# Kernel tuning notes

Hardware: AMD Instinct MI355X
Metric: run time of the kernel (lower is better)

The kernel has to match this reference:

```python
import jax, jax.numpy as jnp
import numpy as np

DIM = 512
HIDDEN = 1024
NUM_EXPERTS = 8
TOP_K = 2
BALANCE_LOSS_WEIGHT = 0.01


def setup_inputs() -> dict:
    key = jax.random.key(0)
    ks = jax.random.split(key, 6)
    B, S = 4, 8192
    x = jax.random.normal(ks[0], (B, S, DIM), dtype=jnp.float32)
    # Linear params (stored already transposed for x @ W convenience)
    scale_in = 1.0 / np.sqrt(DIM)
    scale_hid = 1.0 / np.sqrt(HIDDEN)
    gate_w = jax.random.uniform(ks[1], (DIM, NUM_EXPERTS), jnp.float32, -scale_in, scale_in)
    w1 = jax.random.uniform(ks[2], (NUM_EXPERTS, DIM, HIDDEN), jnp.float32, -scale_in, scale_in)
    b1 = jax.random.uniform(ks[3], (NUM_EXPERTS, HIDDEN), jnp.float32, -scale_in, scale_in)
    w2 = jax.random.uniform(ks[4], (NUM_EXPERTS, HIDDEN, DIM), jnp.float32, -scale_hid, scale_hid)
    b2 = jax.random.uniform(ks[5], (NUM_EXPERTS, DIM), jnp.float32, -scale_hid, scale_hid)
    return {"x": x, "gate_w": gate_w, "w1": w1, "b1": b1, "w2": w2, "b2": b2}


def reference(x, gate_w, w1, b1, w2, b2):
    B, S, D = x.shape
    T = B * S
    E = gate_w.shape[1]
    flat_x = x.reshape(T, D)

    # Gating (eval mode: no noise)
    gate_logits = flat_x @ gate_w                      # [T, E]
    gates = jax.nn.softmax(gate_logits, axis=-1)
    top_k_gates, top_k_indices = jax.lax.top_k(gates, TOP_K)
    top_k_gates = top_k_gates / jnp.sum(top_k_gates, axis=-1, keepdims=True)

    rows = jnp.arange(T)[:, None]
    # Per-token combine weight for each expert (0 if not selected)
    combine_w = jnp.zeros((T, E), flat_x.dtype).at[rows, top_k_indices].add(top_k_gates)
    # Load-balance loss (indices are discrete -> constant mask)
    expert_mask = jnp.zeros((T, E), flat_x.dtype).at[rows, top_k_indices].set(1.0)
    expert_usage = expert_mask.sum(0) / T
    balance_loss = jnp.mean((expert_usage - 1.0 / E) ** 2) * E * BALANCE_LOSS_WEIGHT

    # Expert MLPs; unselected tokens have combine weight 0 so contribute nothing,
    # matching the original masked gather/scatter math exactly.
    out = jnp.zeros_like(flat_x)
    for e in range(E):  # small fixed expert count
        h = jax.nn.gelu(flat_x @ w1[e] + b1[e], approximate=False)  # [T, HIDDEN]
        out = out + (h @ w2[e] + b2[e]) * combine_w[:, e:e + 1]
    return out.reshape(B, S, D), balance_loss
```

## Files before the change

### kernel.cpp

```cpp
#include <hip/hip_runtime.h>
#include <stdint.h>

#define T_TOK 32768
#define DDIM 512
#define HID 1024
#define NEXP 8

typedef _Float16 f16;
typedef _Float16 f16x8 __attribute__((ext_vector_type(8)));
typedef _Float16 f16x4 __attribute__((ext_vector_type(4)));
typedef float f32x4 __attribute__((ext_vector_type(4)));

__device__ __forceinline__ void gload_lds16(const void* g, void* l) {
  __builtin_amdgcn_global_load_lds(
      (__attribute__((address_space(1))) void*)g,
      (__attribute__((address_space(3))) void*)l, 16, 0, 0);
}

__global__ void k_cvt_x(const float* __restrict__ x, f16* __restrict__ xh) {
  int i = blockIdx.x * blockDim.x + threadIdx.x;
  float4 v = ((const float4*)x)[i];
  f16x4 o = {(f16)v.x, (f16)v.y, (f16)v.z, (f16)v.w};
  ((f16x4*)xh)[i] = o;
}

__global__ void k_transpose(const float* __restrict__ W, f16* __restrict__ Wt,
                            const int K, const int N) {
  __shared__ float tile[64][65];
  const int e = blockIdx.z;
  const float* Wb = W + (size_t)e * K * N;
  f16* Wtb = Wt + (size_t)e * K * N;
  const int k0 = blockIdx.x * 64, n0 = blockIdx.y * 64;
  const int tr = threadIdx.x >> 2;
  const int tc = (threadIdx.x & 3) * 16;
#pragma unroll
  for (int j = 0; j < 16; j += 4) {
    float4 v = *(const float4*)&Wb[(size_t)(k0 + tr) * N + n0 + tc + j];
    tile[tr][tc + j + 0] = v.x; tile[tr][tc + j + 1] = v.y;
    tile[tr][tc + j + 2] = v.z; tile[tr][tc + j + 3] = v.w;
  }
  __syncthreads();
  f16x8 t0, t1;
#pragma unroll
  for (int j = 0; j < 8; ++j) {
    t0[j] = (f16)tile[tc + j][tr];
    t1[j] = (f16)tile[tc + 8 + j][tr];
  }
  *(f16x8*)&Wtb[(size_t)(n0 + tr) * K + k0 + tc] = t0;
  *(f16x8*)&Wtb[(size_t)(n0 + tr) * K + k0 + tc + 8] = t1;
}

__global__ void k_gate(const float* __restrict__ x, const float* __restrict__ gw,
                       int* __restrict__ route_e, float* __restrict__ route_w,
                       int* __restrict__ cnt) {
  __shared__ int scnt[NEXP];
  const int tid = threadIdx.x, lane = tid & 63, wv = tid >> 6;
  if (tid < NEXP) scnt[tid] = 0;
  __syncthreads();

  float ga[4][8], gb[4][8];
#pragma unroll
  for (int j = 0; j < 4; ++j) {
    const int r0 = lane * 4 + j;
    const int r1 = 256 + lane * 4 + j;
    float4 q0 = *(const float4*)&gw[r0 * 8];
    float4 q1 = *(const float4*)&gw[r0 * 8 + 4];
    ga[j][0] = q0.x; ga[j][1] = q0.y; ga[j][2] = q0.z; ga[j][3] = q0.w;
    ga[j][4] = q1.x; ga[j][5] = q1.y; ga[j][6] = q1.z; ga[j][7] = q1.w;
    q0 = *(const float4*)&gw[r1 * 8];
    q1 = *(const float4*)&gw[r1 * 8 + 4];
    gb[j][0] = q0.x; gb[j][1] = q0.y; gb[j][2] = q0.z; gb[j][3] = q0.w;
    gb[j][4] = q1.x; gb[j][5] = q1.y; gb[j][6] = q1.z; gb[j][7] = q1.w;
  }

  const int tbase = blockIdx.x * 32 + wv * 8;
  for (int it = 0; it < 8; ++it) {
    const int t = tbase + it;
    const float4 A = *(const float4*)&x[(size_t)t * DDIM + lane * 4];
    const float4 B = *(const float4*)&x[(size_t)t * DDIM + 256 + lane * 4];
    float p[8];
#pragma unroll
    for (int e = 0; e < 8; ++e) {
      p[e] = A.x * ga[0][e] + A.y * ga[1][e] + A.z * ga[2][e] + A.w * ga[3][e] +
             B.x * gb[0][e] + B.y * gb[1][e] + B.z * gb[2][e] + B.w * gb[3][e];
    }
#pragma unroll
    for (int off = 32; off >= 1; off >>= 1) {
#pragma unroll
      for (int e = 0; e < 8; ++e) p[e] += __shfl_xor(p[e], off);
    }
    if (lane == 0) {
      int e1 = 0;
#pragma unroll
      for (int e = 1; e < 8; ++e) if (p[e] > p[e1]) e1 = e;
      int e2 = (e1 == 0) ? 1 : 0;
#pragma unroll
      for (int e = 0; e < 8; ++e) if (e != e1 && p[e] > p[e2]) e2 = e;
      const float wa = 1.0f / (1.0f + expf(p[e2] - p[e1]));
      route_e[t] = e1 | (e2 << 8);
      route_w[t] = wa;
      atomicAdd(&scnt[e1], 1);
      atomicAdd(&scnt[e2], 1);
    }
  }
  __syncthreads();
  if (tid < NEXP) atomicAdd(&cnt[tid], scnt[tid]);
}

__global__ void k_scan(const int* __restrict__ cnt, int* __restrict__ base,
                       int* __restrict__ cursor, float* __restrict__ out_loss) {
  if (threadIdx.x == 0) {
    int b = 0;
    float loss = 0.0f;
    for (int e = 0; e < NEXP; ++e) {
      base[e] = b;
      cursor[e] = b;
      b += cnt[e];
      float u = (float)cnt[e] / (float)T_TOK - 0.125f;
      loss += u * u;
    }
    *out_loss = loss * 0.01f;
  }
}

__global__ void k_scatter(const int* __restrict__ route_e, const float* __restrict__ route_w,
                          int* __restrict__ cursor, int* __restrict__ tok_slot,
                          float* __restrict__ wgt_slot) {
  const int t = blockIdx.x * blockDim.x + threadIdx.x;
  const int lane = threadIdx.x & 63;
  const int re = route_e[t];
  const float wa = route_w[t];
  const int e1 = re & 0xff, e2 = re >> 8;
#pragma unroll
  for (int e = 0; e < NEXP; ++e) {
    unsigned long long m = __ballot(e1 == e);
    if (m) {
      const int leader = __ffsll(m) - 1;
      int b0 = 0;
      if (lane == leader) b0 = atomicAdd(&cursor[e], __popcll(m));
      b0 = __shfl(b0, leader);
      if (e1 == e) {
        const int pos = b0 + __popcll(m & ((1ull << lane) - 1));
        tok_slot[pos] = t;
        wgt_slot[pos] = wa;
      }
    }
    m = __ballot(e2 == e);
    if (m) {
      const int leader = __ffsll(m) - 1;
      int b0 = 0;
      if (lane == leader) b0 = atomicAdd(&cursor[e], __popcll(m));
      b0 = __shfl(b0, leader);
      if (e2 == e) {
        const int pos = b0 + __popcll(m & ((1ull << lane) - 1));
        tok_slot[pos] = t;
        wgt_slot[pos] = 1.0f - wa;
      }
    }
  }
}

#define STAGE_TILE(k0_, As_, Bs_)                                   \
  do {                                                              \
    _Pragma("unroll") for (int i = 0; i < 4; ++i) {                 \
      gload_lds16(aSrc[i] + (k0_), &(As_)[wv * 2048 + i * 512]);    \
      gload_lds16(bSrc[i] + (k0_), &(Bs_)[wv * 2048 + i * 512]);    \
    }                                                               \
  } while (0)

#define COMPUTE_TILE(As_, Bs_)                                                    \
  do {                                                                            \
    _Pragma("unroll") for (int kb = 0; kb < 2; ++kb) {                            \
      f16x8 af[8], bf[4];                                                         \
      _Pragma("unroll") for (int mf = 0; mf < 8; ++mf) {                          \
        const int row = wm * 128 + mf * 16 + l15;                                 \
        af[mf] = *(const f16x8*)&(As_)[row * 64 + (((kb * 4 + g) ^ (row & 7)) * 8)]; \
      }                                                                           \
      _Pragma("unroll") for (int nf = 0; nf < 4; ++nf) {                          \
        const int row = wn * 64 + nf * 16 + l15;                                  \
        bf[nf] = *(const f16x8*)&(Bs_)[row * 64 + (((kb * 4 + g) ^ (row & 7)) * 8)]; \
      }                                                                           \
      _Pragma("unroll") for (int mf = 0; mf < 8; ++mf)                            \
        _Pragma("unroll") for (int nf = 0; nf < 4; ++nf)                          \
          acc[mf][nf] =                                                           \
              __builtin_amdgcn_mfma_f32_16x16x32_f16(af[mf], bf[nf], acc[mf][nf], 0, 0, 0); \
    }                                                                             \
  } while (0)

__global__ __launch_bounds__(512, 2) void k_mlp1(
    const f16* __restrict__ xh, const f16* __restrict__ w1t,
    const float* __restrict__ b1, f16* __restrict__ h,
    const int* __restrict__ tok_slot, const int* __restrict__ base,
    const int* __restrict__ cnt, const int hc, const int c0) {
  const int lid = blockIdx.x;
  const int e = lid & 7;
  const int q = lid >> 3;
  const int mt = q & 63;
  const int nt = q >> 6;
  const int ne = cnt[e];
  const int n0 = nt * 256;
  const int sbase = base[e];
  const int shi = sbase + ne;

  __shared__ f16 As0[256 * 64];
  __shared__ f16 Bs0[256 * 64];
  __shared__ f16 As1[256 * 64];
  __shared__ f16 Bs1[256 * 64];

  const int tid = threadIdx.x;
  const int lane = tid & 63;
  const int wv = tid >> 6;
  const int wm = wv >> 2, wn = wv & 3;
  const int g = lane >> 4;
  const int l15 = lane & 15;

  for (int m0 = mt * 256; m0 < ne; m0 += 64 * 256) {
    const int slot0 = sbase + m0;

    const f16* aSrc[4];
    const f16* bSrc[4];
#pragma unroll
    for (int i = 0; i < 4; ++i) {
      const int row = wv * 32 + i * 8 + (lane >> 3);
      const int sw = ((lane & 7) ^ (lane >> 3)) * 8;
      int slot = slot0 + row;
      slot = (slot <= shi - 1) ? slot : (shi - 1);
      const int tok = tok_slot[slot];
      aSrc[i] = xh + (size_t)tok * DDIM + sw;
      bSrc[i] = w1t + (size_t)(e * HID + c0 + n0 + row) * DDIM + sw;
    }

    f32x4 acc[8][4];
#pragma unroll
    for (int a = 0; a < 8; ++a)
#pragma unroll
      for (int b = 0; b < 4; ++b) { f32x4 z = {0.f, 0.f, 0.f, 0.f}; acc[a][b] = z; }

    const int NT = DDIM / 64;
    STAGE_TILE(0, As0, Bs0);
    __syncthreads();
    for (int t = 0; t < NT; t += 2) {
      if (t + 1 < NT) STAGE_TILE((t + 1) * 64, As1, Bs1);
      COMPUTE_TILE(As0, Bs0);
      __syncthreads();
      if (t + 2 < NT) STAGE_TILE((t + 2) * 64, As0, Bs0);
      COMPUTE_TILE(As1, Bs1);
      __syncthreads();
    }

#pragma unroll
    for (int mf = 0; mf < 8; ++mf) {
#pragma unroll
      for (int r = 0; r < 4; ++r) {
        const int row = wm * 128 + mf * 16 + g * 4 + r;
        const int slot = slot0 + row;
        if (slot >= shi) continue;
#pragma unroll
        for (int nf = 0; nf < 4; ++nf) {
          const int col = wn * 64 + nf * 16 + l15;
          float v = acc[mf][nf][r] + b1[e * HID + c0 + n0 + col];
          v = 0.5f * v * (1.0f + erff(v * 0.70710678118654752f));
          h[(size_t)slot * hc + n0 + col] = (f16)v;
        }
      }
    }
  }
}

__global__ __launch_bounds__(512, 2) void k_mlp2(
    const f16* __restrict__ h, const f16* __restrict__ w2t,
    const float* __restrict__ b2, float* __restrict__ out,
    const int* __restrict__ tok_slot, const float* __restrict__ wgt_slot,
    const int* __restrict__ base, const int* __restrict__ cnt,
    const int hc, const int c0) {
  const int lid = blockIdx.x;
  const int e = lid & 7;
  const int q = lid >> 3;
  const int mt = q & 63;
  const int nt = q >> 6;
  const int ne = cnt[e];
  const int n0 = nt * 256;
  const int sbase = base[e];
  const int shi = sbase + ne;

  __shared__ f16 As0[256 * 64];
  __shared__ f16 Bs0[256 * 64];
  __shared__ f16 As1[256 * 64];
  __shared__ f16 Bs1[256 * 64];

  const int tid = threadIdx.x;
  const int lane = tid & 63;
  const int wv = tid >> 6;
  const int wm = wv >> 2, wn = wv & 3;
  const int g = lane >> 4;
  const int l15 = lane & 15;

  for (int m0 = mt * 256; m0 < ne; m0 += 64 * 256) {
    const int slot0 = sbase + m0;

    const f16* aSrc[4];
    const f16* bSrc[4];
#pragma unroll
    for (int i = 0; i < 4; ++i) {
      const int row = wv * 32 + i * 8 + (lane >> 3);
      const int sw = ((lane & 7) ^ (lane >> 3)) * 8;
      int slot = slot0 + row;
      slot = (slot <= 2 * T_TOK - 1) ? slot : (2 * T_TOK - 1);
      aSrc[i] = h + (size_t)slot * hc + sw;
      bSrc[i] = w2t + (size_t)(e * DDIM + n0 + row) * HID + c0 + sw;
    }

    f32x4 acc[8][4];
#pragma unroll
    for (int a = 0; a < 8; ++a)
#pragma unroll
      for (int b = 0; b < 4; ++b) { f32x4 z = {0.f, 0.f, 0.f, 0.f}; acc[a][b] = z; }

    const int NT = hc / 64;
    STAGE_TILE(0, As0, Bs0);
    __syncthreads();
    for (int t = 0; t < NT; t += 2) {
      if (t + 1 < NT) STAGE_TILE((t + 1) * 64, As1, Bs1);
      COMPUTE_TILE(As0, Bs0);
      __syncthreads();
      if (t + 2 < NT) STAGE_TILE((t + 2) * 64, As0, Bs0);
      COMPUTE_TILE(As1, Bs1);
      __syncthreads();
    }

#pragma unroll
    for (int mf = 0; mf < 8; ++mf) {
#pragma unroll
      for (int r = 0; r < 4; ++r) {
        const int row = wm * 128 + mf * 16 + g * 4 + r;
        const int slot = slot0 + row;
        if (slot >= shi) continue;
        const int tok = tok_slot[slot];
        const float w = wgt_slot[slot];
        float* orow = out + (size_t)tok * DDIM + n0;
#pragma unroll
        for (int nf = 0; nf < 4; ++nf) {
          const int col = wn * 64 + nf * 16 + l15;
          float v = acc[mf][nf][r];
          if (c0 == 0) v += b2[e * DDIM + n0 + col];
          unsafeAtomicAdd(orow + col, w * v);
        }
      }
    }
  }
}

extern "C" void kernel_launch(void* const* d_in, const int* in_sizes, int n_in,
                              void* d_out, int out_size, void* d_ws, size_t ws_size,
                              hipStream_t stream) {
  (void)in_sizes; (void)n_in;
  const float* x  = (const float*)d_in[0];
  const float* gw = (const float*)d_in[1];
  const float* w1 = (const float*)d_in[2];
  const float* b1 = (const float*)d_in[3];
  const float* w2 = (const float*)d_in[4];
  const float* b2 = (const float*)d_in[5];
  float* out = (float*)d_out;

  char* ws = (char*)d_ws;
  size_t off = 0;
  auto alloc = [&](size_t bytes) {
    char* p = ws + off;
    off += (bytes + 255) & ~(size_t)255;
    return p;
  };
  f16*   xh       = (f16*)  alloc((size_t)T_TOK * DDIM * 2);
  f16*   w1t      = (f16*)  alloc((size_t)NEXP * DDIM * HID * 2);
  f16*   w2t      = (f16*)  alloc((size_t)NEXP * DDIM * HID * 2);
  int*   route_e  = (int*)  alloc((size_t)T_TOK * 4);
  float* route_w  = (float*)alloc((size_t)T_TOK * 4);
  int*   tok_slot = (int*)  alloc((size_t)2 * T_TOK * 4);
  float* wgt_slot = (float*)alloc((size_t)2 * T_TOK * 4);
  int*   cnt      = (int*)  alloc(256);
  int*   base     = cnt + 8;
  int*   cursor   = cnt + 16;
  f16*   hbuf     = (f16*)(ws + off);
  const size_t havail = (ws_size > off) ? (ws_size - off) : 0;

  int ns = 4;
  const int cands[3] = {1, 2, 4};
  for (int i = 0; i < 3; ++i) {
    if ((size_t)2 * T_TOK * (HID / cands[i]) * 2 <= havail) { ns = cands[i]; break; }
  }
  const int hc = HID / ns;

  hipMemsetAsync(cnt, 0, 32, stream);
  hipMemsetAsync(d_out, 0, (size_t)out_size * sizeof(float), stream);

  k_cvt_x<<<dim3(T_TOK * DDIM / 4 / 256), 256, 0, stream>>>(x, xh);
  k_transpose<<<dim3(DDIM / 64, HID / 64, NEXP), 256, 0, stream>>>(w1, w1t, DDIM, HID);
  k_transpose<<<dim3(HID / 64, DDIM / 64, NEXP), 256, 0, stream>>>(w2, w2t, HID, DDIM);
  k_gate<<<dim3(T_TOK / 32), 256, 0, stream>>>(x, gw, route_e, route_w, cnt);
  k_scan<<<1, 64, 0, stream>>>(cnt, base, cursor, out + (size_t)T_TOK * DDIM);
  k_scatter<<<dim3(T_TOK / 256), 256, 0, stream>>>(route_e, route_w, cursor, tok_slot, wgt_slot);

  for (int c = 0; c < ns; ++c) {
    k_mlp1<<<dim3(8 * 64 * (hc / 256)), 512, 0, stream>>>(
        xh, w1t, b1, hbuf, tok_slot, base, cnt, hc, c * hc);
    k_mlp2<<<dim3(8 * 64 * 2), 512, 0, stream>>>(
        hbuf, w2t, b2, out, tok_slot, wgt_slot, base, cnt, hc, c * hc);
  }
}
```

Before: 710.4 us.

## Use 4-stage LDS pipeline with BK=32 and fine-grained vmcnt waits in expert GEMMs

Replaces the double-buffered BK=64 GEMM main loop in both expert MLP kernels with a 4-slot ring of BK=32 tiles and three tiles in flight. Each iteration waits only on the oldest tile through explicit s_waitcnt vmcnt counts and one barrier, instead of two full __syncthreads per pair of tiles. The aim is to hide global-load latency and cut synchronisation stalls. The LDS footprint stays at 128KB, and the risks are halving the work per barrier and relying on an exact count of outstanding loads for correctness.

After: 673.6 us. 5.2% less time.

```diff
diff --git a/kernel.cpp b/kernel.cpp
--- a/kernel.cpp
+++ b/kernel.cpp
@@ -5,6 +5,7 @@
 #define DDIM 512
 #define HID 1024
 #define NEXP 8
+#define BKT 32
 
 typedef _Float16 f16;
 typedef _Float16 f16x8 __attribute__((ext_vector_type(8)));
@@ -160,31 +161,53 @@
   }
 }
 
-#define STAGE_TILE(k0_, As_, Bs_)                                   \
-  do {                                                              \
-    _Pragma("unroll") for (int i = 0; i < 4; ++i) {                 \
-      gload_lds16(aSrc[i] + (k0_), &(As_)[wv * 2048 + i * 512]);    \
-      gload_lds16(bSrc[i] + (k0_), &(Bs_)[wv * 2048 + i * 512]);    \
-    }                                                               \
+
+#define STAGE_T(t_)                                                  \
+  do {                                                               \
+    f16* _ldsA = &lds[((t_) & 3) * 16384];                           \
+    f16* _ldsB = _ldsA + 8192;                                       \
+    const int _k = (t_) * BKT;                                       \
+    gload_lds16(aSrc[0] + _k, _ldsA + (wv * 2 + 0) * 512);           \
+    gload_lds16(aSrc[1] + _k, _ldsA + (wv * 2 + 1) * 512);           \
+    gload_lds16(bSrc[0] + _k, _ldsB + (wv * 2 + 0) * 512);           \
+    gload_lds16(bSrc[1] + _k, _ldsB + (wv * 2 + 1) * 512);           \
   } while (0)
 
-#define COMPUTE_TILE(As_, Bs_)                                                    \
+#define COMPUTE_T(t_)                                                             \
   do {                                                                            \
-    _Pragma("unroll") for (int kb = 0; kb < 2; ++kb) {                            \
-      f16x8 af[8], bf[4];                                                         \
-      _Pragma("unroll") for (int mf = 0; mf < 8; ++mf) {                          \
-        const int row = wm * 128 + mf * 16 + l15;                                 \
-        af[mf] = *(const f16x8*)&(As_)[row * 64 + (((kb * 4 + g) ^ (row & 7)) * 8)]; \
-      }                                                                           \
-      _Pragma("unroll") for (int nf = 0; nf < 4; ++nf) {                          \
-        const int row = wn * 64 + nf * 16 + l15;                                  \
-        bf[nf] = *(const f16x8*)&(Bs_)[row * 64 + (((kb * 4 + g) ^ (row & 7)) * 8)]; \
-      }                                                                           \
-      _Pragma("unroll") for (int mf = 0; mf < 8; ++mf)                            \
-        _Pragma("unroll") for (int nf = 0; nf < 4; ++nf)                          \
-          acc[mf][nf] =                                                           \
-              __builtin_amdgcn_mfma_f32_16x16x32_f16(af[mf], bf[nf], acc[mf][nf], 0, 0, 0); \
+    const f16* _A = &lds[((t_) & 3) * 16384];                                     \
+    const f16* _B = _A + 8192;                                                    \
+    f16x8 af[8], bf[4];                                                           \
+    _Pragma("unroll") for (int mf = 0; mf < 8; ++mf) {                            \
+      const int row = wm * 128 + mf * 16 + l15;                                   \
+      af[mf] = *(const f16x8*)&_A[row * 32 + ((g ^ (row & 3)) * 8)];              \
     }                                                                             \
+    _Pragma("unroll") for (int nf = 0; nf < 4; ++nf) {                            \
+      const int row = wn * 64 + nf * 16 + l15;                                    \
+      bf[nf] = *(const f16x8*)&_B[row * 32 + ((g ^ (row & 3)) * 8)];              \
+    }                                                                             \
+    _Pragma("unroll") for (int mf = 0; mf < 8; ++mf)                              \
+      _Pragma("unroll") for (int nf = 0; nf < 4; ++nf)                            \
+        acc[mf][nf] =                                                             \
+            __builtin_amdgcn_mfma_f32_16x16x32_f16(af[mf], bf[nf], acc[mf][nf], 0, 0, 0); \
+  } while (0)
+
+#define PIPE_LOOP(NT_)                                               \
+  do {                                                               \
+    STAGE_T(0); STAGE_T(1); STAGE_T(2);                              \
+    for (int t = 0; t < (NT_); ++t) {                                \
+      const int rem = (NT_)-1 - t;                                   \
+      if (rem >= 2)                                                  \
+        asm volatile("s_waitcnt vmcnt(8)" ::: "memory");             \
+      else if (rem == 1)                                             \
+        asm volatile("s_waitcnt vmcnt(4)" ::: "memory");             \
+      else                                                           \
+        asm volatile("s_waitcnt vmcnt(0)" ::: "memory");             \
+      __builtin_amdgcn_s_barrier();                                  \
+      __builtin_amdgcn_sched_barrier(0);                             \
+      COMPUTE_T(t);                                                  \
+      if (t + 3 < (NT_)) STAGE_T(t + 3);                             \
+    }                                                                \
   } while (0)
 
 __global__ __launch_bounds__(512, 2) void k_mlp1(
@@ -202,10 +225,7 @@
   const int sbase = base[e];
   const int shi = sbase + ne;
 
-  __shared__ f16 As0[256 * 64];
-  __shared__ f16 Bs0[256 * 64];
-  __shared__ f16 As1[256 * 64];
-  __shared__ f16 Bs1[256 * 64];
+  __shared__ f16 lds[4 * 16384];
 
   const int tid = threadIdx.x;
   const int lane = tid & 63;
@@ -213,21 +233,23 @@
   const int wm = wv >> 2, wn = wv & 3;
   const int g = lane >> 4;
   const int l15 = lane & 15;
+  const int lr = lane >> 2;
+  const int lc = lane & 3;
 
   for (int m0 = mt * 256; m0 < ne; m0 += 64 * 256) {
     const int slot0 = sbase + m0;
 
-    const f16* aSrc[4];
-    const f16* bSrc[4];
-#pragma unroll
-    for (int i = 0; i < 4; ++i) {
-      const int row = wv * 32 + i * 8 + (lane >> 3);
-      const int sw = ((lane & 7) ^ (lane >> 3)) * 8;
+    const f16* aSrc[2];
+    const f16* bSrc[2];
+#pragma unroll
+    for (int i = 0; i < 2; ++i) {
+      const int row = (wv * 2 + i) * 16 + lr;
+      const int ch = lc ^ (row & 3);
       int slot = slot0 + row;
       slot = (slot <= shi - 1) ? slot : (shi - 1);
       const int tok = tok_slot[slot];
-      aSrc[i] = xh + (size_t)tok * DDIM + sw;
-      bSrc[i] = w1t + (size_t)(e * HID + c0 + n0 + row) * DDIM + sw;
+      aSrc[i] = xh + (size_t)tok * DDIM + ch * 8;
+      bSrc[i] = w1t + (size_t)(e * HID + c0 + n0 + row) * DDIM + ch * 8;
     }
 
     f32x4 acc[8][4];
@@ -236,17 +258,7 @@
 #pragma unroll
       for (int b = 0; b < 4; ++b) { f32x4 z = {0.f, 0.f, 0.f, 0.f}; acc[a][b] = z; }
 
-    const int NT = DDIM / 64;
-    STAGE_TILE(0, As0, Bs0);
-    __syncthreads();
-    for (int t = 0; t < NT; t += 2) {
-      if (t + 1 < NT) STAGE_TILE((t + 1) * 64, As1, Bs1);
-      COMPUTE_TILE(As0, Bs0);
-      __syncthreads();
-      if (t + 2 < NT) STAGE_TILE((t + 2) * 64, As0, Bs0);
-      COMPUTE_TILE(As1, Bs1);
-      __syncthreads();
-    }
+    PIPE_LOOP(DDIM / BKT);
 
 #pragma unroll
     for (int mf = 0; mf < 8; ++mf) {
@@ -283,10 +295,7 @@
   const int sbase = base[e];
   const int shi = sbase + ne;
 
-  __shared__ f16 As0[256 * 64];
-  __shared__ f16 Bs0[256 * 64];
-  __shared__ f16 As1[256 * 64];
-  __shared__ f16 Bs1[256 * 64];
+  __shared__ f16 lds[4 * 16384];
 
   const int tid = threadIdx.x;
   const int lane = tid & 63;
@@ -294,20 +303,22 @@
   const int wm = wv >> 2, wn = wv & 3;
   const int g = lane >> 4;
   const int l15 = lane & 15;
+  const int lr = lane >> 2;
+  const int lc = lane & 3;
 
   for (int m0 = mt * 256; m0 < ne; m0 += 64 * 256) {
     const int slot0 = sbase + m0;
 
-    const f16* aSrc[4];
-    const f16* bSrc[4];
-#pragma unroll
-    for (int i = 0; i < 4; ++i) {
-      const int row = wv * 32 + i * 8 + (lane >> 3);
-      const int sw = ((lane & 7) ^ (lane >> 3)) * 8;
+    const f16* aSrc[2];
+    const f16* bSrc[2];
+#pragma unroll
+    for (int i = 0; i < 2; ++i) {
+      const int row = (wv * 2 + i) * 16 + lr;
+      const int ch = lc ^ (row & 3);
       int slot = slot0 + row;
       slot = (slot <= 2 * T_TOK - 1) ? slot : (2 * T_TOK - 1);
-      aSrc[i] = h + (size_t)slot * hc + sw;
-      bSrc[i] = w2t + (size_t)(e * DDIM + n0 + row) * HID + c0 + sw;
+      aSrc[i] = h + (size_t)slot * hc + ch * 8;
+      bSrc[i] = w2t + (size_t)(e * DDIM + n0 + row) * HID + c0 + ch * 8;
     }
 
     f32x4 acc[8][4];
@@ -316,17 +327,7 @@
 #pragma unroll
       for (int b = 0; b < 4; ++b) { f32x4 z = {0.f, 0.f, 0.f, 0.f}; acc[a][b] = z; }
 
-    const int NT = hc / 64;
-    STAGE_TILE(0, As0, Bs0);
-    __syncthreads();
-    for (int t = 0; t < NT; t += 2) {
-      if (t + 1 < NT) STAGE_TILE((t + 1) * 64, As1, Bs1);
-      COMPUTE_TILE(As0, Bs0);
-      __syncthreads();
-      if (t + 2 < NT) STAGE_TILE((t + 2) * 64, As0, Bs0);
-      COMPUTE_TILE(As1, Bs1);
-      __syncthreads();
-    }
+    PIPE_LOOP(hc / BKT);
 
 #pragma unroll
     for (int mf = 0; mf < 8; ++mf) {
```
